# Kernel tuning notes

Measured on AMD Instinct MI355X. Metric: run time of the kernel, lower is better.

## Reference

```python
import jax, jax.numpy as jnp
import numpy as np

B, N, D = 32, 4096, 256      # batch, num input features, input dim
S, H, M = 11, 256, 512       # num_slots, slot_size, mlp_hidden_size
ITERS = 3
ATTN_EPS = 1e-8
LN_EPS = 1e-5


def layer_norm(x, scale, offset):
    mu = jnp.mean(x, axis=-1, keepdims=True)
    var = jnp.var(x, axis=-1, keepdims=True)
    return (x - mu) * scale * jax.lax.rsqrt(var + LN_EPS) + offset


def gru_unroll(updates, w_i, w_h, b):
    # haiku hk.GRU unrolled over axis 1 (time_major=False), zero initial state.
    # updates: [B, T, H]
    h0 = jnp.zeros((updates.shape[0], H), updates.dtype)
    def step(h, x):
        gx = jnp.matmul(x, w_i)                                    # [B, 3H]
        zr = jax.nn.sigmoid(gx[:, :2 * H] + jnp.matmul(h, w_h[:, :2 * H]) + b[:2 * H])
        z, r = zr[:, :H], zr[:, H:]
        a = jnp.tanh(gx[:, 2 * H:] + jnp.matmul(r * h, w_h[:, 2 * H:]) + b[2 * H:])
        h_new = (1.0 - z) * h + z * a
        return h_new, h_new
    _, outs = jax.lax.scan(step, h0, jnp.swapaxes(updates, 0, 1))
    return jnp.swapaxes(outs, 0, 1)                                # [B, T, H]


def setup_inputs():
    key = jax.random.key(0)
    k = jax.random.split(key, 16)
    def lin(kk, fan_in, fan_out):
        return jax.random.normal(kk, (fan_in, fan_out), jnp.float32) / np.sqrt(fan_in).astype(np.float32)
    return {
        "inputs": jax.random.normal(k[0], (B, N, D), jnp.float32),
        "slot_noise": jax.random.normal(k[1], (B, S, H), jnp.float32),
        "ln_in_scale": jnp.ones((D,), jnp.float32),
        "ln_in_offset": jnp.zeros((D,), jnp.float32),
        "ln_slots_scale": jnp.ones((H,), jnp.float32),
        "ln_slots_offset": jnp.zeros((H,), jnp.float32),
        "ln_mlp_scale": jnp.ones((H,), jnp.float32),
        "ln_mlp_offset": jnp.zeros((H,), jnp.float32),
        "slots_mu": jax.random.normal(k[2], (1, 1, H), jnp.float32) * 0.1,
        "slots_log_sigma": jax.random.normal(k[3], (1, 1, H), jnp.float32) * 0.1 - 1.0,
        "Wq": lin(k[4], H, H),
        "Wk": lin(k[5], D, H),
        "Wv": lin(k[6], D, H),
        "gru_wi": lin(k[7], H, 3 * H),
        "gru_wh": lin(k[8], H, 3 * H),
        "gru_b": jnp.zeros((3 * H,), jnp.float32),
        "mlp_w1": lin(k[9], H, M),
        "mlp_b1": jnp.zeros((M,), jnp.float32),
        "mlp_w2": lin(k[10], M, H),
        "mlp_b2": jnp.zeros((H,), jnp.float32),
    }


def reference(inputs, slot_noise, ln_in_scale, ln_in_offset, ln_slots_scale,
              ln_slots_offset, ln_mlp_scale, ln_mlp_offset, slots_mu,
              slots_log_sigma, Wq, Wk, Wv, gru_wi, gru_wh, gru_b,
              mlp_w1, mlp_b1, mlp_w2, mlp_b2):
    x = layer_norm(inputs, ln_in_scale, ln_in_offset)
    kf = jnp.matmul(x, Wk)                                          # [B, N, H]
    vf = jnp.matmul(x, Wv)                                          # [B, N, H]
    slots = slots_mu + jnp.exp(slots_log_sigma) * slot_noise        # [B, S, H]
    scale = H ** (-0.5)
    for _ in range(ITERS):
        q = jnp.matmul(layer_norm(slots, ln_slots_scale, ln_slots_offset), Wq) * scale
        attn_logits = jnp.einsum('bnh,bsh->bns', kf, q)             # [B, N, S]
        attn = jax.nn.softmax(attn_logits, axis=-1) + ATTN_EPS      # softmax over slots
        attn = attn / jnp.sum(attn, axis=-2, keepdims=True)         # normalize over inputs
        updates = jnp.einsum('bns,bnh->bsh', attn, vf)              # [B, S, H]
        slots = gru_unroll(updates, gru_wi, gru_wh, gru_b)          # GRU over slot axis
        mlp_in = layer_norm(slots, ln_mlp_scale, ln_mlp_offset)
        hid = jax.nn.relu(jnp.matmul(mlp_in, mlp_w1) + mlp_b1)
        slots = slots + jnp.matmul(hid, mlp_w2) + mlp_b2
    return slots
```

## Files before the change

kernel.cpp:

```cpp
#include <hip/hip_runtime.h>

typedef unsigned short u16;
typedef __bf16 bf16x8 __attribute__((ext_vector_type(8)));
typedef float  f32x4  __attribute__((ext_vector_type(4)));
typedef unsigned short u16x8 __attribute__((ext_vector_type(8)));

union U8cast { u16x8 u; bf16x8 b; };

#define NB 32
#define NN 4096
#define ND 256
#define NS 11
#define NH 256
#define NM 512

__device__ __forceinline__ u16 f2bf(float f) {
  unsigned u = __float_as_uint(f);
  u += 0x7FFF + ((u >> 16) & 1);
  return (u16)(u >> 16);
}
__device__ __forceinline__ float bf2f(u16 h) {
  return __uint_as_float(((unsigned)h) << 16);
}

__global__ void k_stats(const float* __restrict__ x, float2* __restrict__ mu_rs) {
  int lane = threadIdx.x & 63;
  int wid  = threadIdx.x >> 6;
  int row  = blockIdx.x * 4 + wid;
  float4 v = *(const float4*)(x + (size_t)row * 256 + lane * 4);
  float s1 = v.x + v.y + v.z + v.w;
  float s2 = v.x*v.x + v.y*v.y + v.z*v.z + v.w*v.w;
#pragma unroll
  for (int off = 32; off; off >>= 1) { s1 += __shfl_xor(s1, off); s2 += __shfl_xor(s2, off); }
  if (lane == 0) {
    float mu  = s1 * (1.f/256.f);
    float var = s2 * (1.f/256.f) - mu*mu;
    mu_rs[row] = make_float2(mu, rsqrtf(var + 1e-5f));
  }
}

__global__ __launch_bounds__(256)
void k_cvt_w(const float* __restrict__ Wk, const float* __restrict__ Wv,
             u16* __restrict__ wT) {
  __shared__ float Lt[64][65];
  int bx = blockIdx.x;
  int kt = bx & 3, ct = bx >> 2;
  int k0 = kt * 64, c0 = ct * 64;
  const float* src = (c0 < 256) ? Wk : Wv;
  int c0m = c0 & 255;
  int t = threadIdx.x;
  int kr = t >> 2, part = t & 3;
  const float* sp = src + (size_t)(k0 + kr) * 256 + c0m + part * 16;
#pragma unroll
  for (int g = 0; g < 4; ++g) {
    float4 v = *(const float4*)(sp + g * 4);
    Lt[kr][part*16 + g*4 + 0] = v.x;
    Lt[kr][part*16 + g*4 + 1] = v.y;
    Lt[kr][part*16 + g*4 + 2] = v.z;
    Lt[kr][part*16 + g*4 + 3] = v.w;
  }
  __syncthreads();
  int cr = t >> 2;
  u16* wp = wT + (size_t)(c0 + cr) * 256 + k0 + part * 16;
#pragma unroll
  for (int g = 0; g < 2; ++g) {
    u16x8 o;
#pragma unroll
    for (int j = 0; j < 8; ++j) o[j] = f2bf(Lt[part*16 + g*8 + j][cr]);
    *(u16x8*)(wp + g * 8) = o;
  }
}

__global__ void k_cvt_all(const float* __restrict__ Wq, const float* __restrict__ wi,
                          const float* __restrict__ wh, const float* __restrict__ w1,
                          const float* __restrict__ w2, u16* __restrict__ wqb,
                          u16* __restrict__ wib, u16* __restrict__ whb,
                          u16* __restrict__ w1b, u16* __restrict__ w2b) {
  int idx = blockIdx.x * 256 + threadIdx.x;
  if      (idx < 65536)  wqb[idx]          = f2bf(Wq[idx]);
  else if (idx < 262144) wib[idx - 65536]  = f2bf(wi[idx - 65536]);
  else if (idx < 458752) whb[idx - 262144] = f2bf(wh[idx - 262144]);
  else if (idx < 589824) w1b[idx - 458752] = f2bf(w1[idx - 458752]);
  else                   w2b[idx - 589824] = f2bf(w2[idx - 589824]);
}

__global__ void k_slots_init(const float* __restrict__ noise, const float* __restrict__ mu,
                             const float* __restrict__ ls, float* __restrict__ slots) {
  int row = blockIdx.x, t = threadIdx.x;
  slots[row*256 + t] = mu[t] + expf(ls[t]) * noise[row*256 + t];
}

__global__ __launch_bounds__(256)
void k_gemm_kv(const float* __restrict__ x, const float2* __restrict__ mu_rs,
               const float* __restrict__ lnsc, const float* __restrict__ lnof,
               const u16* __restrict__ wT, u16* __restrict__ kv) {
  __shared__ __align__(16) u16 Al[128][72];
  __shared__ __align__(16) u16 Bl[128][72];
  __shared__ float scl[256], ofl[256];
  int t = threadIdx.x;
  scl[t] = lnsc[t]; ofl[t] = lnof[t];

  int bid = blockIdx.x;
  int xcd  = bid & 7;
  int slot = bid >> 3;
  int colt = slot & 3;
  int rowt = xcd * 128 + (slot >> 2);
  int row0 = rowt * 128;
  int col0 = colt * 128;

  int srow = t >> 1, shalf = t & 1;
  float2 mr = mu_rs[row0 + srow];
  int lane = t & 63, w = t >> 6;
  int wm = (w & 1) * 64, wn = (w >> 1) * 64;
  int fr = lane & 15;
  int kq = (lane >> 4) * 8;
  f32x4 acc[4][4] = {};
  const float* xp0 = x + (size_t)(row0 + srow) * 256 + shalf * 32;
  for (int kc = 0; kc < 256; kc += 64) {
    __syncthreads();
    {
      const float* xp = xp0 + kc;
#pragma unroll
      for (int g = 0; g < 4; ++g) {
        float4 f0 = *(const float4*)(xp + g*8);
        float4 f1 = *(const float4*)(xp + g*8 + 4);
        int kb = kc + shalf*32 + g*8;
        bf16x8 o;
        o[0] = (__bf16)((f0.x - mr.x) * (mr.y * scl[kb+0]) + ofl[kb+0]);
        o[1] = (__bf16)((f0.y - mr.x) * (mr.y * scl[kb+1]) + ofl[kb+1]);
        o[2] = (__bf16)((f0.z - mr.x) * (mr.y * scl[kb+2]) + ofl[kb+2]);
        o[3] = (__bf16)((f0.w - mr.x) * (mr.y * scl[kb+3]) + ofl[kb+3]);
        o[4] = (__bf16)((f1.x - mr.x) * (mr.y * scl[kb+4]) + ofl[kb+4]);
        o[5] = (__bf16)((f1.y - mr.x) * (mr.y * scl[kb+5]) + ofl[kb+5]);
        o[6] = (__bf16)((f1.z - mr.x) * (mr.y * scl[kb+6]) + ofl[kb+6]);
        o[7] = (__bf16)((f1.w - mr.x) * (mr.y * scl[kb+7]) + ofl[kb+7]);
        *(bf16x8*)&Al[srow][shalf*32 + g*8] = o;
      }
      const u16* wp = wT + (size_t)(col0 + srow) * 256 + kc + shalf*32;
#pragma unroll
      for (int g = 0; g < 4; ++g)
        *(u16x8*)&Bl[srow][shalf*32 + g*8] = *(const u16x8*)(wp + g*8);
    }
    __syncthreads();
#pragma unroll
    for (int ks = 0; ks < 2; ++ks) {
      int kk = ks*32 + kq;
      bf16x8 af[4], bfr[4];
#pragma unroll
      for (int i = 0; i < 4; ++i) af[i] = *(const bf16x8*)&Al[wm + i*16 + fr][kk];
#pragma unroll
      for (int i = 0; i < 4; ++i) bfr[i] = *(const bf16x8*)&Bl[wn + i*16 + fr][kk];
#pragma unroll
      for (int im = 0; im < 4; ++im)
#pragma unroll
        for (int in = 0; in < 4; ++in)
          acc[im][in] = __builtin_amdgcn_mfma_f32_16x16x32_bf16(af[im], bfr[in], acc[im][in], 0, 0, 0);
    }
  }
  int r4 = (lane >> 4) * 4;
#pragma unroll
  for (int im = 0; im < 4; ++im)
#pragma unroll
    for (int in = 0; in < 4; ++in) {
      int gcol = col0 + wn + in*16 + fr;
#pragma unroll
      for (int r = 0; r < 4; ++r) {
        int grow = row0 + wm + im*16 + r4 + r;
        kv[(size_t)grow * 512 + gcol] = f2bf(acc[im][in][r]);
      }
    }
}

__global__ __launch_bounds__(256)
void k_q_ln(const float* __restrict__ slots, const float* __restrict__ sc,
            const float* __restrict__ of, const u16* __restrict__ wqb,
            float* __restrict__ q, float* __restrict__ updates,
            float* __restrict__ colsum) {
  __shared__ float xn[256];
  __shared__ float red[8];
  __shared__ float part[8][256];
  int row = blockIdx.x, t = threadIdx.x;
  float v = slots[row*256 + t];
  float s1 = v, s2 = v*v;
#pragma unroll
  for (int off = 32; off; off >>= 1) { s1 += __shfl_xor(s1, off); s2 += __shfl_xor(s2, off); }
  int w = t >> 6;
  if ((t & 63) == 0) { red[w*2] = s1; red[w*2+1] = s2; }
  __syncthreads();
  float a1 = red[0] + red[2] + red[4] + red[6];
  float a2 = red[1] + red[3] + red[5] + red[7];
  float mu = a1 * (1.f/256.f);
  float rs = rsqrtf(a2 * (1.f/256.f) - mu*mu + 1e-5f);
  xn[t] = (v - mu) * rs * sc[t] + of[t];
  updates[row*256 + t] = 0.f;
  if (t == 0) colsum[(row/11)*16 + (row%11)] = 0.f;
  __syncthreads();
  int tc = t & 31, kg = t >> 5;
  float a[8] = {};
#pragma unroll 8
  for (int kk = 0; kk < 32; ++kk) {
    int k = kg*32 + kk;
    float xv = xn[k];
    u16x8 wv = *(const u16x8*)(wqb + k*256 + tc*8);
#pragma unroll
    for (int j = 0; j < 8; ++j) a[j] += xv * bf2f(wv[j]);
  }
  *(float4*)&part[kg][tc*8]     = make_float4(a[0], a[1], a[2], a[3]);
  *(float4*)&part[kg][tc*8 + 4] = make_float4(a[4], a[5], a[6], a[7]);
  __syncthreads();
  float s = 0.f;
#pragma unroll
  for (int g = 0; g < 8; ++g) s += part[g][t];
  q[row*256 + t] = s * 0.0625f;
}

__global__ __launch_bounds__(256)
void k_attn_up(const u16* __restrict__ kv, const float* __restrict__ qg,
               float* __restrict__ updates, float* __restrict__ colsum) {
  __shared__ __align__(16) u16 kfL[64][264];
  __shared__ __align__(16) u16 vfL[64][256];
  __shared__ __align__(16) u16 qTL[16][264];
  __shared__ __align__(16) u16 PTL[16][72];
  __shared__ float Lg[64][17];
  int t = threadIdx.x;
  int b = blockIdx.y;
  int nb0 = blockIdx.x * 256;
  int lane = t & 63, w = t >> 6;
  int fr = lane & 15, kq = lane >> 4;

#pragma unroll
  for (int i = t; i < 512; i += 256) {
    int s = i >> 5, k0 = (i & 31) * 8;
    u16x8 o;
    if (s < 11) {
      const float* qp = qg + (size_t)b*2816 + s*256 + k0;
#pragma unroll
      for (int j = 0; j < 8; ++j) o[j] = f2bf(qp[j]);
    } else {
#pragma unroll
      for (int j = 0; j < 8; ++j) o[j] = 0;
    }
    *(u16x8*)&qTL[s][k0] = o;
  }
  for (int i = t; i < 16*72; i += 256) ((u16*)PTL)[i] = 0;

  f32x4 accU[4] = {};
  float csA[11];
#pragma unroll
  for (int s = 0; s < 11; ++s) csA[s] = 0.f;

  for (int c = 0; c < 4; ++c) {
    int n0 = nb0 + c*64;
    __syncthreads();
    {
      int hc = (t & 31) * 8;
#pragma unroll
      for (int nr = 0; nr < 8; ++nr) {
        int n = nr*8 + (t >> 5);
        size_t base = ((size_t)b*4096 + n0 + n) * 512;
        u16x8 kvk = *(const u16x8*)(kv + base + hc);
        *(u16x8*)&kfL[n][hc] = kvk;
        u16x8 kvv = *(const u16x8*)(kv + base + 256 + hc);
        *(u16x8*)&vfL[n][hc ^ (((n >> 3) & 3) * 16)] = kvv;
      }
    }
    __syncthreads();
    {
      f32x4 aL = {};
#pragma unroll
      for (int kc = 0; kc < 256; kc += 32) {
        bf16x8 af = *(const bf16x8*)&kfL[w*16 + fr][kc + kq*8];
        bf16x8 bq = *(const bf16x8*)&qTL[fr][kc + kq*8];
        aL = __builtin_amdgcn_mfma_f32_16x16x32_bf16(af, bq, aL, 0, 0, 0);
      }
#pragma unroll
      for (int r = 0; r < 4; ++r)
        Lg[w*16 + kq*4 + r][fr] = aL[r];
    }
    __syncthreads();
    if (t < 64) {
      float p[11];
#pragma unroll
      for (int s = 0; s < 11; ++s) p[s] = Lg[t][s];
      float m = p[0];
#pragma unroll
      for (int s = 1; s < 11; ++s) m = fmaxf(m, p[s]);
      float Z = 0.f;
#pragma unroll
      for (int s = 0; s < 11; ++s) { p[s] = __expf(p[s] - m); Z += p[s]; }
      float iz = 1.f / Z;
#pragma unroll
      for (int s = 0; s < 11; ++s) {
        u16 pb = f2bf(p[s]*iz + 1e-8f);
        csA[s] += bf2f(pb);
        PTL[s][t] = pb;
      }
    }
    __syncthreads();
#pragma unroll
    for (int ht = 0; ht < 4; ++ht) {
      int h = w*64 + ht*16 + fr;
#pragma unroll
      for (int kc = 0; kc < 64; kc += 32) {
        bf16x8 aP = *(const bf16x8*)&PTL[fr][kc + kq*8];
        U8cast bv;
#pragma unroll
        for (int j = 0; j < 8; ++j) {
          int k = kc + kq*8 + j;
          bv.u[j] = vfL[k][h ^ (((k >> 3) & 3) * 16)];
        }
        accU[ht] = __builtin_amdgcn_mfma_f32_16x16x32_bf16(aP, bv.b, accU[ht], 0, 0, 0);
      }
    }
  }
#pragma unroll
  for (int ht = 0; ht < 4; ++ht) {
    int h = w*64 + ht*16 + fr;
#pragma unroll
    for (int r = 0; r < 4; ++r) {
      int s = kq*4 + r;
      if (s < 11)
        atomicAdd(&updates[((size_t)b*11 + s)*256 + h], accU[ht][r]);
    }
  }
  if (t < 64) {
#pragma unroll
    for (int s = 0; s < 11; ++s) {
#pragma unroll
      for (int off = 32; off; off >>= 1) csA[s] += __shfl_xor(csA[s], off);
    }
    if (lane == 0) {
#pragma unroll
      for (int s = 0; s < 11; ++s) atomicAdd(&colsum[b*16 + s], csA[s]);
    }
  }
}

__global__ __launch_bounds__(384)
void k_gx(const float* __restrict__ updates, const float* __restrict__ colsum,
          const u16* __restrict__ wib, float* __restrict__ gx) {
  __shared__ float xn[256];
  __shared__ float part[4][768];
  int row = blockIdx.x, t = threadIdx.x;
  if (t < 256) {
    float inv = 1.f / colsum[(row/11)*16 + (row%11)];
    xn[t] = updates[row*256 + t] * inv;
  }
  __syncthreads();
  int tc = t % 96, kg = t / 96;
  float a[8] = {};
#pragma unroll 4
  for (int kk = 0; kk < 64; ++kk) {
    int k = kg*64 + kk;
    float xv = xn[k];
    u16x8 wv = *(const u16x8*)(wib + k*768 + tc*8);
#pragma unroll
    for (int j = 0; j < 8; ++j) a[j] += xv * bf2f(wv[j]);
  }
  *(float4*)&part[kg][tc*8]     = make_float4(a[0], a[1], a[2], a[3]);
  *(float4*)&part[kg][tc*8 + 4] = make_float4(a[4], a[5], a[6], a[7]);
  __syncthreads();
#pragma unroll
  for (int c = t; c < 768; c += 384) {
    float s = part[0][c] + part[1][c] + part[2][c] + part[3][c];
    gx[row*768 + c] = s;
  }
}

__global__ __launch_bounds__(512)
void k_gru(const float* __restrict__ gx, const u16* __restrict__ whb,
           const float* __restrict__ gb, float* __restrict__ slots) {
  __shared__ float h[256], rh[256], zv[256];
  __shared__ float part[4096];
  int b = blockIdx.x, t = threadIdx.x;
  if (t < 256) h[t] = 0.f;
  __syncthreads();
  for (int step = 0; step < 11; ++step) {
    int row = b*11 + step;
    {
      int tc = t & 63, kg = t >> 6;
      float a[8] = {};
#pragma unroll 8
      for (int kk = 0; kk < 32; ++kk) {
        int k = kg*32 + kk;
        float xv = h[k];
        u16x8 wv = *(const u16x8*)(whb + k*768 + tc*8);
#pragma unroll
        for (int j = 0; j < 8; ++j) a[j] += xv * bf2f(wv[j]);
      }
      *(float4*)&part[kg*512 + tc*8]     = make_float4(a[0], a[1], a[2], a[3]);
      *(float4*)&part[kg*512 + tc*8 + 4] = make_float4(a[4], a[5], a[6], a[7]);
    }
    __syncthreads();
    {
      int c = t;
      float s = gx[row*768 + c] + gb[c];
#pragma unroll
      for (int g = 0; g < 8; ++g) s += part[g*512 + c];
      float sg = 1.f / (1.f + __expf(-s));
      if (c < 256) zv[c] = sg;
      else         rh[c - 256] = sg * h[c - 256];
    }
    __syncthreads();
    {
      int tc = t & 31, kg = t >> 5;
      float a[8] = {};
#pragma unroll 8
      for (int kk = 0; kk < 16; ++kk) {
        int k = kg*16 + kk;
        float xv = rh[k];
        u16x8 wv = *(const u16x8*)(whb + k*768 + 512 + tc*8);
#pragma unroll
        for (int j = 0; j < 8; ++j) a[j] += xv * bf2f(wv[j]);
      }
      *(float4*)&part[kg*256 + tc*8]     = make_float4(a[0], a[1], a[2], a[3]);
      *(float4*)&part[kg*256 + tc*8 + 4] = make_float4(a[4], a[5], a[6], a[7]);
    }
    __syncthreads();
    if (t < 256) {
      int c = t;
      float s = gx[row*768 + 512 + c] + gb[512 + c];
#pragma unroll
      for (int g = 0; g < 16; ++g) s += part[g*256 + c];
      float av = tanhf(s);
      float hn = (1.f - zv[c])*h[c] + zv[c]*av;
      h[c] = hn;
      slots[row*256 + c] = hn;
    }
    __syncthreads();
  }
}

__global__ __launch_bounds__(256)
void k_mlp(float* __restrict__ slots, const float* __restrict__ sc,
           const float* __restrict__ of, const u16* __restrict__ w1b,
           const float* __restrict__ b1, const u16* __restrict__ w2b,
           const float* __restrict__ b2, float* __restrict__ out2) {
  __shared__ float xn[256];
  __shared__ float hid[512];
  __shared__ float red[8];
  __shared__ float part[2048];
  int row = blockIdx.x, t = threadIdx.x;
  float v = slots[row*256 + t];
  float s1 = v, s2 = v*v;
#pragma unroll
  for (int off = 32; off; off >>= 1) { s1 += __shfl_xor(s1, off); s2 += __shfl_xor(s2, off); }
  int w = t >> 6;
  if ((t & 63) == 0) { red[w*2] = s1; red[w*2+1] = s2; }
  __syncthreads();
  float a1s = red[0] + red[2] + red[4] + red[6];
  float a2s = red[1] + red[3] + red[5] + red[7];
  float mu = a1s * (1.f/256.f);
  float rs = rsqrtf(a2s * (1.f/256.f) - mu*mu + 1e-5f);
  xn[t] = (v - mu) * rs * sc[t] + of[t];
  __syncthreads();
  {
    int tc = t & 63, kg = t >> 6;
    float a[8] = {};
#pragma unroll 4
    for (int kk = 0; kk < 64; ++kk) {
      int k = kg*64 + kk;
      float xv = xn[k];
      u16x8 wv = *(const u16x8*)(w1b + k*512 + tc*8);
#pragma unroll
      for (int j = 0; j < 8; ++j) a[j] += xv * bf2f(wv[j]);
    }
    *(float4*)&part[kg*512 + tc*8]     = make_float4(a[0], a[1], a[2], a[3]);
    *(float4*)&part[kg*512 + tc*8 + 4] = make_float4(a[4], a[5], a[6], a[7]);
  }
  __syncthreads();
#pragma unroll
  for (int c = t; c < 512; c += 256) {
    float s = b1[c];
#pragma unroll
    for (int g = 0; g < 4; ++g) s += part[g*512 + c];
    hid[c] = fmaxf(s, 0.f);
  }
  __syncthreads();
  {
    int tc = t & 31, kg = t >> 5;
    float a[8] = {};
#pragma unroll 4
    for (int kk = 0; kk < 64; ++kk) {
      int k = kg*64 + kk;
      float xv = hid[k];
      u16x8 wv = *(const u16x8*)(w2b + k*256 + tc*8);
#pragma unroll
      for (int j = 0; j < 8; ++j) a[j] += xv * bf2f(wv[j]);
    }
    *(float4*)&part[kg*256 + tc*8]     = make_float4(a[0], a[1], a[2], a[3]);
    *(float4*)&part[kg*256 + tc*8 + 4] = make_float4(a[4], a[5], a[6], a[7]);
  }
  __syncthreads();
  {
    float s = v + b2[t];
#pragma unroll
    for (int g = 0; g < 8; ++g) s += part[g*256 + t];
    slots[row*256 + t] = s;
    if (out2) out2[row*256 + t] = s;
  }
}

extern "C" void kernel_launch(void* const* d_in, const int* in_sizes, int n_in,
                              void* d_out, int out_size, void* d_ws, size_t ws_size,
                              hipStream_t stream) {
  (void)in_sizes; (void)n_in; (void)out_size; (void)ws_size;
  const float* inputs = (const float*)d_in[0];
  const float* noise  = (const float*)d_in[1];
  const float* lnin_s = (const float*)d_in[2];
  const float* lnin_o = (const float*)d_in[3];
  const float* lnsl_s = (const float*)d_in[4];
  const float* lnsl_o = (const float*)d_in[5];
  const float* lnml_s = (const float*)d_in[6];
  const float* lnml_o = (const float*)d_in[7];
  const float* smu    = (const float*)d_in[8];
  const float* sls    = (const float*)d_in[9];
  const float* Wq     = (const float*)d_in[10];
  const float* Wk     = (const float*)d_in[11];
  const float* Wv     = (const float*)d_in[12];
  const float* gwi    = (const float*)d_in[13];
  const float* gwh    = (const float*)d_in[14];
  const float* gb     = (const float*)d_in[15];
  const float* w1     = (const float*)d_in[16];
  const float* b1     = (const float*)d_in[17];
  const float* w2     = (const float*)d_in[18];
  const float* b2     = (const float*)d_in[19];

  char* ws = (char*)d_ws;
  u16*    kv      = (u16*)(ws);
  u16*    wT      = (u16*)(ws + 134217728);
  float2* mu_rs   = (float2*)(ws + 134479872);
  float*  slots   = (float*)(ws + 139984896);
  float*  updates = (float*)(ws + 140345344);
  float*  gx      = (float*)(ws + 140705792);
  float*  q       = (float*)(ws + 140705792);
  float*  colsum  = (float*)(ws + 141787136);
  u16*    wqb     = (u16*)(ws + 141789184);
  u16*    wib     = (u16*)(ws + 141920256);
  u16*    whb     = (u16*)(ws + 142313472);
  u16*    w1b     = (u16*)(ws + 142706688);
  u16*    w2b     = (u16*)(ws + 142968832);

  k_stats     <<<32768, 256, 0, stream>>>(inputs, mu_rs);
  k_cvt_w     <<<32,    256, 0, stream>>>(Wk, Wv, wT);
  k_cvt_all   <<<2816,  256, 0, stream>>>(Wq, gwi, gwh, w1, w2, wqb, wib, whb, w1b, w2b);
  k_slots_init<<<352,   256, 0, stream>>>(noise, smu, sls, slots);
  k_gemm_kv   <<<4096,  256, 0, stream>>>(inputs, mu_rs, lnin_s, lnin_o, wT, kv);

  for (int it = 0; it < 3; ++it) {
    k_q_ln    <<<352, 256, 0, stream>>>(slots, lnsl_s, lnsl_o, wqb, q, updates, colsum);
    k_attn_up <<<dim3(16, 32), 256, 0, stream>>>(kv, q, updates, colsum);
    k_gx      <<<352, 384, 0, stream>>>(updates, colsum, wib, gx);
    k_gru     <<<32,  512, 0, stream>>>(gx, whb, gb, slots);
    k_mlp     <<<352, 256, 0, stream>>>(slots, lnml_s, lnml_o, w1b, b1, w2b, b2,
                                        (it == 2) ? (float*)d_out : nullptr);
  }
}
```

Before: 659.7 us.

## Pre-normalize inputs to bf16 and use direct global-to-LDS loads in KV GEMM

The stats kernel now applies the input layer norm itself and writes a bf16 copy of the normalized inputs. A new KV GEMM reads that bf16 buffer with global_load_lds into swizzled shared memory, so it no longer normalizes and converts fp32 inputs inside the GEMM. This halves the GEMM's input reads and simplifies its load path. The cost is an extra 64MB bf16 write and read-back, and the fast path only runs when the workspace is large enough.

New measurement: 615.7 us. -6.7%, faster.

```diff
diff --git a/kernel.cpp b/kernel.cpp
--- a/kernel.cpp
+++ b/kernel.cpp
@@ -21,6 +21,11 @@
 }
 __device__ __forceinline__ float bf2f(u16 h) {
   return __uint_as_float(((unsigned)h) << 16);
+}
+
+__device__ __forceinline__ void gload_lds16(const void* g, void* l) {
+  __builtin_amdgcn_global_load_lds((const __attribute__((address_space(1))) void*)g,
+                                   (__attribute__((address_space(3))) void*)l, 16, 0, 0);
 }
 
 __global__ void k_stats(const float* __restrict__ x, float2* __restrict__ mu_rs) {
@@ -37,6 +42,28 @@
     float var = s2 * (1.f/256.f) - mu*mu;
     mu_rs[row] = make_float2(mu, rsqrtf(var + 1e-5f));
   }
+}
+
+__global__ void k_stats_ln(const float* __restrict__ x, const float* __restrict__ sc,
+                           const float* __restrict__ of, u16* __restrict__ xbf) {
+  int lane = threadIdx.x & 63;
+  int wid  = threadIdx.x >> 6;
+  int row  = blockIdx.x * 4 + wid;
+  float4 v = *(const float4*)(x + (size_t)row * 256 + lane * 4);
+  float s1 = v.x + v.y + v.z + v.w;
+  float s2 = v.x*v.x + v.y*v.y + v.z*v.z + v.w*v.w;
+#pragma unroll
+  for (int off = 32; off; off >>= 1) { s1 += __shfl_xor(s1, off); s2 += __shfl_xor(s2, off); }
+  float mu = s1 * (1.f/256.f);
+  float rs = rsqrtf(s2 * (1.f/256.f) - mu*mu + 1e-5f);
+  float4 s4 = *(const float4*)(sc + lane * 4);
+  float4 o4 = *(const float4*)(of + lane * 4);
+  ushort4 o;
+  o.x = f2bf((v.x - mu) * (rs * s4.x) + o4.x);
+  o.y = f2bf((v.y - mu) * (rs * s4.y) + o4.y);
+  o.z = f2bf((v.z - mu) * (rs * s4.z) + o4.z);
+  o.w = f2bf((v.w - mu) * (rs * s4.w) + o4.w);
+  *(ushort4*)(xbf + (size_t)row * 256 + lane * 4) = o;
 }
 
 __global__ __launch_bounds__(256)
@@ -88,6 +115,75 @@
                              const float* __restrict__ ls, float* __restrict__ slots) {
   int row = blockIdx.x, t = threadIdx.x;
   slots[row*256 + t] = mu[t] + expf(ls[t]) * noise[row*256 + t];
+}
+
+__global__ __launch_bounds__(256)
+void k_gemm_kv_fast(const u16* __restrict__ xbf, const u16* __restrict__ wT,
+                    u16* __restrict__ kv) {
+  __shared__ __align__(16) u16 Al[128 * 64];
+  __shared__ __align__(16) u16 Bl[128 * 64];
+  int t = threadIdx.x;
+  int bid = blockIdx.x;
+  int xcd  = bid & 7;
+  int slot = bid >> 3;
+  int colt = slot & 3;
+  int rowt = xcd * 128 + (slot >> 2);
+  int row0 = rowt * 128;
+  int col0 = colt * 128;
+
+  int lane = t & 63, w = t >> 6;
+  int wm = (w & 1) * 64, wn = (w >> 1) * 64;
+  int fr = lane & 15, kq = lane >> 4;
+
+  int srow = w * 8 + (lane >> 3);
+  int k2   = (((lane & 7) ^ ((lane >> 3) & 7)) << 4);
+  const u16* agp = xbf + (size_t)(row0 + srow) * 256 + (k2 >> 1);
+  const u16* bgp = wT  + (size_t)(col0 + srow) * 256 + (k2 >> 1);
+  u16* Alw = Al + w * 512;
+  u16* Blw = Bl + w * 512;
+
+  f32x4 acc[4][4] = {};
+  for (int kc = 0; kc < 256; kc += 64) {
+    __syncthreads();
+#pragma unroll
+    for (int i = 0; i < 4; ++i) {
+      gload_lds16(agp + (size_t)i * 32 * 256 + kc, Alw + i * 2048);
+      gload_lds16(bgp + (size_t)i * 32 * 256 + kc, Blw + i * 2048);
+    }
+    __syncthreads();
+#pragma unroll
+    for (int ks = 0; ks < 2; ++ks) {
+      int kb = ks * 64 + kq * 16;
+      bf16x8 af[4], bfr[4];
+#pragma unroll
+      for (int i = 0; i < 4; ++i) {
+        int row = wm + i * 16 + fr;
+        af[i] = *(const bf16x8*)((const char*)Al + row * 128 + (kb ^ ((fr & 7) << 4)));
+      }
+#pragma unroll
+      for (int i = 0; i < 4; ++i) {
+        int row = wn + i * 16 + fr;
+        bfr[i] = *(const bf16x8*)((const char*)Bl + row * 128 + (kb ^ ((fr & 7) << 4)));
+      }
+#pragma unroll
+      for (int im = 0; im < 4; ++im)
+#pragma unroll
+        for (int in = 0; in < 4; ++in)
+          acc[im][in] = __builtin_amdgcn_mfma_f32_16x16x32_bf16(af[im], bfr[in], acc[im][in], 0, 0, 0);
+    }
+  }
+  int r4 = kq * 4;
+#pragma unroll
+  for (int im = 0; im < 4; ++im)
+#pragma unroll
+    for (int in = 0; in < 4; ++in) {
+      int gcol = col0 + wn + in*16 + fr;
+#pragma unroll
+      for (int r = 0; r < 4; ++r) {
+        int grow = row0 + wm + im*16 + r4 + r;
+        kv[(size_t)grow * 512 + gcol] = f2bf(acc[im][in][r]);
+      }
+    }
 }
 
 __global__ __launch_bounds__(256)
@@ -504,7 +600,7 @@
 extern "C" void kernel_launch(void* const* d_in, const int* in_sizes, int n_in,
                               void* d_out, int out_size, void* d_ws, size_t ws_size,
                               hipStream_t stream) {
-  (void)in_sizes; (void)n_in; (void)out_size; (void)ws_size;
+  (void)in_sizes; (void)n_in; (void)out_size;
   const float* inputs = (const float*)d_in[0];
   const float* noise  = (const float*)d_in[1];
   const float* lnin_s = (const float*)d_in[2];
@@ -540,12 +636,24 @@
   u16*    whb     = (u16*)(ws + 142313472);
   u16*    w1b     = (u16*)(ws + 142706688);
   u16*    w2b     = (u16*)(ws + 142968832);
-
-  k_stats     <<<32768, 256, 0, stream>>>(inputs, mu_rs);
+  u16*    xbf     = (u16*)(ws + 143230976);
+  const size_t WS_FAST = 143230976ull + 67108864ull;
+
+  int fast = (ws_size == 0 || ws_size >= WS_FAST) ? 1 : 0;
+
+  if (fast) {
+    k_stats_ln<<<32768, 256, 0, stream>>>(inputs, lnin_s, lnin_o, xbf);
+  } else {
+    k_stats   <<<32768, 256, 0, stream>>>(inputs, mu_rs);
+  }
   k_cvt_w     <<<32,    256, 0, stream>>>(Wk, Wv, wT);
   k_cvt_all   <<<2816,  256, 0, stream>>>(Wq, gwi, gwh, w1, w2, wqb, wib, whb, w1b, w2b);
   k_slots_init<<<352,   256, 0, stream>>>(noise, smu, sls, slots);
-  k_gemm_kv   <<<4096,  256, 0, stream>>>(inputs, mu_rs, lnin_s, lnin_o, wT, kv);
+  if (fast) {
+    k_gemm_kv_fast<<<4096, 256, 0, stream>>>(xbf, wT, kv);
+  } else {
+    k_gemm_kv     <<<4096, 256, 0, stream>>>(inputs, mu_rs, lnin_s, lnin_o, wT, kv);
+  }
 
   for (int it = 0; it < 3; ++it) {
     k_q_ln    <<<352, 256, 0, stream>>>(slots, lnsl_s, lnsl_o, wqb, q, updates, colsum);
```

## Fold Wk into query projection and compute logits directly against normalized inputs

Applied to the files above, without the earlier changes.

Removes the key projection GEMM by precomputing M = Wq·Wkᵀ, so each iteration's query becomes LN(slots)·M and the attention logits are taken directly against the layer-normalized bf16 inputs. The input layernorm is materialized once as bf16, and the remaining value GEMM now reads bf16 tiles via direct global-to-LDS loads with double buffering and an XOR swizzle. This halves the projection GEMM work and the kv write traffic. In exchange it adds a bf16 xbf buffer write and a different rounding path for the logits, since M is rounded to bf16 and built from already bf16-rounded Wk.

New measurement: 585.5 us. -11.2%, faster.

```diff
diff --git a/kernel.cpp b/kernel.cpp
--- a/kernel.cpp
+++ b/kernel.cpp
@@ -23,7 +23,13 @@
   return __uint_as_float(((unsigned)h) << 16);
 }
 
-__global__ void k_stats(const float* __restrict__ x, float2* __restrict__ mu_rs) {
+__device__ __forceinline__ void gload_lds16(const void* g, void* l) {
+  __builtin_amdgcn_global_load_lds((const __attribute__((address_space(1))) void*)g,
+                                   (__attribute__((address_space(3))) void*)l, 16, 0, 0);
+}
+
+__global__ void k_stats_ln(const float* __restrict__ x, const float* __restrict__ sc,
+                           const float* __restrict__ of, u16* __restrict__ xbf) {
   int lane = threadIdx.x & 63;
   int wid  = threadIdx.x >> 6;
   int row  = blockIdx.x * 4 + wid;
@@ -32,11 +38,16 @@
   float s2 = v.x*v.x + v.y*v.y + v.z*v.z + v.w*v.w;
 #pragma unroll
   for (int off = 32; off; off >>= 1) { s1 += __shfl_xor(s1, off); s2 += __shfl_xor(s2, off); }
-  if (lane == 0) {
-    float mu  = s1 * (1.f/256.f);
-    float var = s2 * (1.f/256.f) - mu*mu;
-    mu_rs[row] = make_float2(mu, rsqrtf(var + 1e-5f));
-  }
+  float mu = s1 * (1.f/256.f);
+  float rs = rsqrtf(s2 * (1.f/256.f) - mu*mu + 1e-5f);
+  float4 s4 = *(const float4*)(sc + lane * 4);
+  float4 o4 = *(const float4*)(of + lane * 4);
+  ushort4 o;
+  o.x = f2bf((v.x - mu) * (rs * s4.x) + o4.x);
+  o.y = f2bf((v.y - mu) * (rs * s4.y) + o4.y);
+  o.z = f2bf((v.z - mu) * (rs * s4.z) + o4.z);
+  o.w = f2bf((v.w - mu) * (rs * s4.w) + o4.w);
+  *(ushort4*)(xbf + (size_t)row * 256 + lane * 4) = o;
 }
 
 __global__ __launch_bounds__(256)
@@ -71,93 +82,120 @@
   }
 }
 
-__global__ void k_cvt_all(const float* __restrict__ Wq, const float* __restrict__ wi,
-                          const float* __restrict__ wh, const float* __restrict__ w1,
-                          const float* __restrict__ w2, u16* __restrict__ wqb,
+__global__ __launch_bounds__(256)
+void k_mk(const float* __restrict__ Wq, const u16* __restrict__ wT,
+          u16* __restrict__ Mb) {
+  __shared__ float xn[256];
+  __shared__ float part[8][256];
+  int e = blockIdx.x, t = threadIdx.x;
+  xn[t] = Wq[e*256 + t];
+  __syncthreads();
+  int tc = t & 31, kg = t >> 5;
+  float a[8] = {};
+#pragma unroll 8
+  for (int kk = 0; kk < 32; ++kk) {
+    int k = kg*32 + kk;
+    float xv = xn[k];
+    u16x8 wv = *(const u16x8*)(wT + k*256 + tc*8);
+#pragma unroll
+    for (int j = 0; j < 8; ++j) a[j] += xv * bf2f(wv[j]);
+  }
+  *(float4*)&part[kg][tc*8]     = make_float4(a[0], a[1], a[2], a[3]);
+  *(float4*)&part[kg][tc*8 + 4] = make_float4(a[4], a[5], a[6], a[7]);
+  __syncthreads();
+  float s = 0.f;
+#pragma unroll
+  for (int g = 0; g < 8; ++g) s += part[g][t];
+  Mb[e*256 + t] = f2bf(s);
+}
+
+__global__ void k_cvt_all(const float* __restrict__ wi, const float* __restrict__ wh,
+                          const float* __restrict__ w1, const float* __restrict__ w2,
+                          const float* __restrict__ noise, const float* __restrict__ smu,
+                          const float* __restrict__ sls,
                           u16* __restrict__ wib, u16* __restrict__ whb,
-                          u16* __restrict__ w1b, u16* __restrict__ w2b) {
+                          u16* __restrict__ w1b, u16* __restrict__ w2b,
+                          float* __restrict__ slots) {
   int idx = blockIdx.x * 256 + threadIdx.x;
-  if      (idx < 65536)  wqb[idx]          = f2bf(Wq[idx]);
-  else if (idx < 262144) wib[idx - 65536]  = f2bf(wi[idx - 65536]);
-  else if (idx < 458752) whb[idx - 262144] = f2bf(wh[idx - 262144]);
-  else if (idx < 589824) w1b[idx - 458752] = f2bf(w1[idx - 458752]);
-  else                   w2b[idx - 589824] = f2bf(w2[idx - 589824]);
-}
-
-__global__ void k_slots_init(const float* __restrict__ noise, const float* __restrict__ mu,
-                             const float* __restrict__ ls, float* __restrict__ slots) {
-  int row = blockIdx.x, t = threadIdx.x;
-  slots[row*256 + t] = mu[t] + expf(ls[t]) * noise[row*256 + t];
+  if      (idx < 196608) wib[idx]          = f2bf(wi[idx]);
+  else if (idx < 393216) whb[idx - 196608] = f2bf(wh[idx - 196608]);
+  else if (idx < 524288) w1b[idx - 393216] = f2bf(w1[idx - 393216]);
+  else if (idx < 655360) w2b[idx - 524288] = f2bf(w2[idx - 524288]);
+  else {
+    int i = idx - 655360;
+    int c = i & 255;
+    slots[i] = smu[c] + expf(sls[c]) * noise[i];
+  }
 }
 
 __global__ __launch_bounds__(256)
-void k_gemm_kv(const float* __restrict__ x, const float2* __restrict__ mu_rs,
-               const float* __restrict__ lnsc, const float* __restrict__ lnof,
-               const u16* __restrict__ wT, u16* __restrict__ kv) {
-  __shared__ __align__(16) u16 Al[128][72];
-  __shared__ __align__(16) u16 Bl[128][72];
-  __shared__ float scl[256], ofl[256];
+void k_gemm_vf(const u16* __restrict__ xbf, const u16* __restrict__ wTv,
+               u16* __restrict__ vf) {
+  __shared__ __align__(16) u16 Al[2][128 * 64];
+  __shared__ __align__(16) u16 Bl[2][128 * 64];
   int t = threadIdx.x;
-  scl[t] = lnsc[t]; ofl[t] = lnof[t];
-
   int bid = blockIdx.x;
   int xcd  = bid & 7;
   int slot = bid >> 3;
-  int colt = slot & 3;
-  int rowt = xcd * 128 + (slot >> 2);
+  int colt = slot & 1;
+  int rowt = xcd * 128 + (slot >> 1);
   int row0 = rowt * 128;
   int col0 = colt * 128;
 
-  int srow = t >> 1, shalf = t & 1;
-  float2 mr = mu_rs[row0 + srow];
   int lane = t & 63, w = t >> 6;
   int wm = (w & 1) * 64, wn = (w >> 1) * 64;
-  int fr = lane & 15;
-  int kq = (lane >> 4) * 8;
+  int fr = lane & 15, kq = lane >> 4;
+
+  int srow = w * 8 + (lane >> 3);
+  int k2   = (((lane & 7) ^ ((lane >> 3) & 7)) << 4);
+  const u16* agp = xbf + (size_t)(row0 + srow) * 256 + (k2 >> 1);
+  const u16* bgp = wTv + (size_t)(col0 + srow) * 256 + (k2 >> 1);
+
   f32x4 acc[4][4] = {};
-  const float* xp0 = x + (size_t)(row0 + srow) * 256 + shalf * 32;
-  for (int kc = 0; kc < 256; kc += 64) {
-    __syncthreads();
-    {
-      const float* xp = xp0 + kc;
-#pragma unroll
-      for (int g = 0; g < 4; ++g) {
-        float4 f0 = *(const float4*)(xp + g*8);
-        float4 f1 = *(const float4*)(xp + g*8 + 4);
-        int kb = kc + shalf*32 + g*8;
-        bf16x8 o;
-        o[0] = (__bf16)((f0.x - mr.x) * (mr.y * scl[kb+0]) + ofl[kb+0]);
-        o[1] = (__bf16)((f0.y - mr.x) * (mr.y * scl[kb+1]) + ofl[kb+1]);
-        o[2] = (__bf16)((f0.z - mr.x) * (mr.y * scl[kb+2]) + ofl[kb+2]);
-        o[3] = (__bf16)((f0.w - mr.x) * (mr.y * scl[kb+3]) + ofl[kb+3]);
-        o[4] = (__bf16)((f1.x - mr.x) * (mr.y * scl[kb+4]) + ofl[kb+4]);
-        o[5] = (__bf16)((f1.y - mr.x) * (mr.y * scl[kb+5]) + ofl[kb+5]);
-        o[6] = (__bf16)((f1.z - mr.x) * (mr.y * scl[kb+6]) + ofl[kb+6]);
-        o[7] = (__bf16)((f1.w - mr.x) * (mr.y * scl[kb+7]) + ofl[kb+7]);
-        *(bf16x8*)&Al[srow][shalf*32 + g*8] = o;
-      }
-      const u16* wp = wT + (size_t)(col0 + srow) * 256 + kc + shalf*32;
-#pragma unroll
-      for (int g = 0; g < 4; ++g)
-        *(u16x8*)&Bl[srow][shalf*32 + g*8] = *(const u16x8*)(wp + g*8);
-    }
-    __syncthreads();
+
+#define STAGE_VF(buf, kc)                                              \
+  {                                                                    \
+    u16* Aw = &Al[buf][w * 512];                                       \
+    u16* Bw = &Bl[buf][w * 512];                                       \
+    _Pragma("unroll")                                                  \
+    for (int i = 0; i < 4; ++i) {                                      \
+      gload_lds16(agp + (size_t)i * 32 * 256 + (kc), Aw + i * 2048);   \
+      gload_lds16(bgp + (size_t)i * 32 * 256 + (kc), Bw + i * 2048);   \
+    }                                                                  \
+  }
+
+  STAGE_VF(0, 0);
+  __syncthreads();
+#pragma unroll
+  for (int t4 = 0; t4 < 4; ++t4) {
+    if (t4 < 3) STAGE_VF((t4 + 1) & 1, (t4 + 1) * 64);
+    const u16* Ab = Al[t4 & 1];
+    const u16* Bb = Bl[t4 & 1];
 #pragma unroll
     for (int ks = 0; ks < 2; ++ks) {
-      int kk = ks*32 + kq;
+      int kb = ks * 64 + kq * 16;
       bf16x8 af[4], bfr[4];
 #pragma unroll
-      for (int i = 0; i < 4; ++i) af[i] = *(const bf16x8*)&Al[wm + i*16 + fr][kk];
-#pragma unroll
-      for (int i = 0; i < 4; ++i) bfr[i] = *(const bf16x8*)&Bl[wn + i*16 + fr][kk];
+      for (int i = 0; i < 4; ++i) {
+        int row = wm + i * 16 + fr;
+        af[i] = *(const bf16x8*)((const char*)Ab + row * 128 + (kb ^ ((fr & 7) << 4)));
+      }
+#pragma unroll
+      for (int i = 0; i < 4; ++i) {
+        int row = wn + i * 16 + fr;
+        bfr[i] = *(const bf16x8*)((const char*)Bb + row * 128 + (kb ^ ((fr & 7) << 4)));
+      }
 #pragma unroll
       for (int im = 0; im < 4; ++im)
 #pragma unroll
         for (int in = 0; in < 4; ++in)
           acc[im][in] = __builtin_amdgcn_mfma_f32_16x16x32_bf16(af[im], bfr[in], acc[im][in], 0, 0, 0);
     }
-  }
-  int r4 = (lane >> 4) * 4;
+    __syncthreads();
+  }
+#undef STAGE_VF
+
+  int r4 = kq * 4;
 #pragma unroll
   for (int im = 0; im < 4; ++im)
 #pragma unroll
@@ -166,15 +204,15 @@
 #pragma unroll
       for (int r = 0; r < 4; ++r) {
         int grow = row0 + wm + im*16 + r4 + r;
-        kv[(size_t)grow * 512 + gcol] = f2bf(acc[im][in][r]);
+        vf[(size_t)grow * 256 + gcol] = f2bf(acc[im][in][r]);
       }
     }
 }
 
 __global__ __launch_bounds__(256)
 void k_q_ln(const float* __restrict__ slots, const float* __restrict__ sc,
-            const float* __restrict__ of, const u16* __restrict__ wqb,
-            float* __restrict__ q, float* __restrict__ updates,
+            const float* __restrict__ of, const u16* __restrict__ Mb,
+            float* __restrict__ qk2, float* __restrict__ updates,
             float* __restrict__ colsum) {
   __shared__ float xn[256];
   __shared__ float red[8];
@@ -201,7 +239,7 @@
   for (int kk = 0; kk < 32; ++kk) {
     int k = kg*32 + kk;
     float xv = xn[k];
-    u16x8 wv = *(const u16x8*)(wqb + k*256 + tc*8);
+    u16x8 wv = *(const u16x8*)(Mb + k*256 + tc*8);
 #pragma unroll
     for (int j = 0; j < 8; ++j) a[j] += xv * bf2f(wv[j]);
   }
@@ -211,11 +249,12 @@
   float s = 0.f;
 #pragma unroll
   for (int g = 0; g < 8; ++g) s += part[g][t];
-  q[row*256 + t] = s * 0.0625f;
+  qk2[row*256 + t] = s * 0.0625f;
 }
 
 __global__ __launch_bounds__(256)
-void k_attn_up(const u16* __restrict__ kv, const float* __restrict__ qg,
+void k_attn_up(const u16* __restrict__ xbf, const u16* __restrict__ vf,
+               const float* __restrict__ qg,
                float* __restrict__ updates, float* __restrict__ colsum) {
   __shared__ __align__(16) u16 kfL[64][264];
   __shared__ __align__(16) u16 vfL[64][256];
@@ -257,10 +296,10 @@
 #pragma unroll
       for (int nr = 0; nr < 8; ++nr) {
         int n = nr*8 + (t >> 5);
-        size_t base = ((size_t)b*4096 + n0 + n) * 512;
-        u16x8 kvk = *(const u16x8*)(kv + base + hc);
+        size_t base = ((size_t)b*4096 + n0 + n) * 256;
+        u16x8 kvk = *(const u16x8*)(xbf + base + hc);
         *(u16x8*)&kfL[n][hc] = kvk;
-        u16x8 kvv = *(const u16x8*)(kv + base + 256 + hc);
+        u16x8 kvv = *(const u16x8*)(vf + base + hc);
         *(u16x8*)&vfL[n][hc ^ (((n >> 3) & 3) * 16)] = kvv;
       }
     }
@@ -527,29 +566,30 @@
   const float* b2     = (const float*)d_in[19];
 
   char* ws = (char*)d_ws;
-  u16*    kv      = (u16*)(ws);
+  u16*    vf      = (u16*)(ws);
   u16*    wT      = (u16*)(ws + 134217728);
-  float2* mu_rs   = (float2*)(ws + 134479872);
   float*  slots   = (float*)(ws + 139984896);
   float*  updates = (float*)(ws + 140345344);
   float*  gx      = (float*)(ws + 140705792);
-  float*  q       = (float*)(ws + 140705792);
+  float*  qk2     = (float*)(ws + 140705792);
   float*  colsum  = (float*)(ws + 141787136);
-  u16*    wqb     = (u16*)(ws + 141789184);
+  u16*    Mb      = (u16*)(ws + 141789184);
   u16*    wib     = (u16*)(ws + 141920256);
   u16*    whb     = (u16*)(ws + 142313472);
   u16*    w1b     = (u16*)(ws + 142706688);
   u16*    w2b     = (u16*)(ws + 142968832);
-
-  k_stats     <<<32768, 256, 0, stream>>>(inputs, mu_rs);
-  k_cvt_w     <<<32,    256, 0, stream>>>(Wk, Wv, wT);
-  k_cvt_all   <<<2816,  256, 0, stream>>>(Wq, gwi, gwh, w1, w2, wqb, wib, whb, w1b, w2b);
-  k_slots_init<<<352,   256, 0, stream>>>(noise, smu, sls, slots);
-  k_gemm_kv   <<<4096,  256, 0, stream>>>(inputs, mu_rs, lnin_s, lnin_o, wT, kv);
+  u16*    xbf     = (u16*)(ws + 143230976);
+
+  k_stats_ln <<<32768, 256, 0, stream>>>(inputs, lnin_s, lnin_o, xbf);
+  k_cvt_w    <<<32,    256, 0, stream>>>(Wk, Wv, wT);
+  k_mk       <<<256,   256, 0, stream>>>(Wq, wT, Mb);
+  k_cvt_all  <<<2912,  256, 0, stream>>>(gwi, gwh, w1, w2, noise, smu, sls,
+                                         wib, whb, w1b, w2b, slots);
+  k_gemm_vf  <<<2048,  256, 0, stream>>>(xbf, wT + 65536, vf);
 
   for (int it = 0; it < 3; ++it) {
-    k_q_ln    <<<352, 256, 0, stream>>>(slots, lnsl_s, lnsl_o, wqb, q, updates, colsum);
-    k_attn_up <<<dim3(16, 32), 256, 0, stream>>>(kv, q, updates, colsum);
+    k_q_ln    <<<352, 256, 0, stream>>>(slots, lnsl_s, lnsl_o, Mb, qk2, updates, colsum);
+    k_attn_up <<<dim3(16, 32), 256, 0, stream>>>(xbf, vf, qk2, updates, colsum);
     k_gx      <<<352, 384, 0, stream>>>(updates, colsum, wib, gx);
     k_gru     <<<32,  512, 0, stream>>>(gx, whb, gb, slots);
     k_mlp     <<<352, 256, 0, stream>>>(slots, lnml_s, lnml_o, w1b, b1, w2b, b2,
```
